# Optimization experiments

Hardware: AMD Instinct MI355X
Metric: run time of the kernel (lower is better)

The kernel has to match this reference:

```python
import jax, jax.numpy as jnp
import numpy as np

C = 1024        # BIGNET_DIM
GS = 128        # group_size
R = 4           # lora_dim
NL = 12         # 4 blocks x 3 QLoRALinear
N = 4096        # batch
NG = C * C // GS  # 8192 groups per layer
EPS = 1e-5


def dequant4(q4, norm):
    # q4: [NG, GS//2] int32 in [0,255] (two nibbles per byte), norm: [NG,1] f32
    low = q4 & 0xF
    high = (q4 >> 4) & 0xF
    # interleave: even positions = low nibble, odd = high nibble
    q8 = jnp.stack([low, high], axis=-1).reshape(q4.shape[0], GS)
    w = (q8.astype(jnp.float32) / 15.0 * 2.0 - 1.0) * norm
    return w.reshape(C, C)  # [out_features, in_features]


def qlora_linear(x, q4, norm, a, b):
    # base 4-bit dequant matmul + low-rank LoRA add (bias=False)
    w = dequant4(q4, norm)
    return x @ w.T + (x @ a.T) @ b.T  # [N,C]


def block(x, q4s, norms, As, Bs):
    h = qlora_linear(x, q4s[0], norms[0], As[0], Bs[0])
    h = jax.nn.relu(h)
    h = qlora_linear(h, q4s[1], norms[1], As[1], Bs[1])
    h = jax.nn.relu(h)
    h = qlora_linear(h, q4s[2], norms[2], As[2], Bs[2])
    return h + x  # residual


def layer_norm(x, g, b):
    mu = jnp.mean(x, axis=-1, keepdims=True)
    var = jnp.var(x, axis=-1, keepdims=True)
    return (x - mu) * jax.lax.rsqrt(var + EPS) * g + b


def setup_inputs() -> dict:
    key = jax.random.key(0)
    ks = jax.random.split(key, 5)
    x = jax.random.normal(ks[0], (N, C), dtype=jnp.float32)
    w_q4 = jax.random.randint(ks[1], (NL, NG, GS // 2), 0, 256, dtype=jnp.int32)
    w_norm = jax.random.uniform(ks[2], (NL, NG, 1), dtype=jnp.float32, minval=0.01, maxval=0.1)
    lora_a = jax.random.normal(ks[3], (NL, R, C), dtype=jnp.float32) * 0.02
    lora_b = jax.random.normal(ks[4], (NL, C, R), dtype=jnp.float32) * 0.02
    ln_g = jnp.ones((2, C), dtype=jnp.float32)
    ln_b = jnp.zeros((2, C), dtype=jnp.float32)
    return {"x": x, "w_q4": w_q4, "w_norm": w_norm, "lora_a": lora_a,
            "lora_b": lora_b, "ln_g": ln_g, "ln_b": ln_b}


def reference(x, w_q4, w_norm, lora_a, lora_b, ln_g, ln_b):
    h = block(x, w_q4[0:3], w_norm[0:3], lora_a[0:3], lora_b[0:3])
    h = layer_norm(h, ln_g[0], ln_b[0])
    h = block(h, w_q4[3:6], w_norm[3:6], lora_a[3:6], lora_b[3:6])
    h = block(h, w_q4[6:9], w_norm[6:9], lora_a[6:9], lora_b[6:9])
    h = layer_norm(h, ln_g[1], ln_b[1])
    h = block(h, w_q4[9:12], w_norm[9:12], lora_a[9:12], lora_b[9:12])
    return h
```

## Files before the change

### kernel.cpp

```cpp
#include <hip/hip_runtime.h>

#define CD 1024
#define NB 4096

typedef __attribute__((ext_vector_type(8))) short short8;
typedef __attribute__((ext_vector_type(4))) short short4v;
typedef __attribute__((ext_vector_type(4))) float f32x4;
typedef __attribute__((ext_vector_type(4))) int int4v;

typedef __attribute__((address_space(1))) const void gv_t;
typedef __attribute__((address_space(3))) void lv_t;
#define GLOAD16(g, l) __builtin_amdgcn_global_load_lds((gv_t*)(g), (lv_t*)(l), 16, 0, 0)

__device__ __forceinline__ short f2bf(float f) {
  unsigned u = __float_as_uint(f);
  u = (u + 0x7FFFu + ((u >> 16) & 1u)) >> 16;
  return (short)u;
}
__device__ __forceinline__ float bf2f(short s) {
  return __uint_as_float(((unsigned)(unsigned short)s) << 16);
}

__global__ __launch_bounds__(256) void prep_kernel(const float* __restrict__ x,
                                                   short* __restrict__ xb,
                                                   const int* __restrict__ q4,
                                                   const float* __restrict__ nrm,
                                                   const float* __restrict__ la,
                                                   const float* __restrict__ lb,
                                                   short* __restrict__ Wb) {
  int bid = blockIdx.x;
  if (bid < 2048) {
    int i = (bid * 256 + threadIdx.x) * 8;
    f32x4 a = *(const f32x4*)(x + i);
    f32x4 b = *(const f32x4*)(x + i + 4);
    short8 o;
    o[0] = f2bf(a[0]); o[1] = f2bf(a[1]); o[2] = f2bf(a[2]); o[3] = f2bf(a[3]);
    o[4] = f2bf(b[0]); o[5] = f2bf(b[1]); o[6] = f2bf(b[2]); o[7] = f2bf(b[3]);
    *(short8*)(xb + i) = o;
    return;
  }
  int tidg = (bid - 2048) * 256 + threadIdx.x;
  int w0 = tidg * 4;
  int l = w0 >> 19;
  int wl = w0 & 524287;
  int g = wl >> 6;
  int j0 = wl & 63;
  int o = g >> 3;
  int kb = ((g & 7) << 7) + (j0 << 1);
  int4v q = *(const int4v*)(q4 + w0);
  float n = nrm[(l << 13) + g];
  float s = n * (2.0f / 15.0f);
  f32x4 B = *(const f32x4*)(lb + (((l << 10) + o) << 2));
  const float* A = la + (l << 12);
  float Ar[4][8];
#pragma unroll
  for (int r = 0; r < 4; ++r) {
    f32x4 u = *(const f32x4*)(A + r * CD + kb);
    f32x4 v = *(const f32x4*)(A + r * CD + kb + 4);
    Ar[r][0] = u[0]; Ar[r][1] = u[1]; Ar[r][2] = u[2]; Ar[r][3] = u[3];
    Ar[r][4] = v[0]; Ar[r][5] = v[1]; Ar[r][6] = v[2]; Ar[r][7] = v[3];
  }
  short8 outv;
#pragma unroll
  for (int p = 0; p < 8; ++p) {
    int qw = q[p >> 1];
    int nib = (qw >> ((p & 1) << 2)) & 15;
    float wv = (float)nib * s - n;
    wv += B[0] * Ar[0][p] + B[1] * Ar[1][p] + B[2] * Ar[2][p] + B[3] * Ar[3][p];
    outv[p] = f2bf(wv);
  }
  *(short8*)(Wb + (l << 20) + (o << 10) + kb) = outv;
}

template <int EPI>
__global__ __launch_bounds__(256, 2) void qgemm(const short* __restrict__ Act,
                                                const short* __restrict__ W,
                                                const short* __restrict__ Res,
                                                void* __restrict__ Out) {
  __shared__ __align__(16) short ldsA[2][128 * 64];
  __shared__ __align__(16) short ldsB[2][64 * 64];
  const int tid = threadIdx.x;
  const int lane = tid & 63;
  const int wid = tid >> 6;
  const int wr = wid >> 1, wc = wid & 1;
  const int m0 = blockIdx.x * 128;
  const int o0 = blockIdx.y * 64;

  const int srow = tid >> 3;
  const int gch = (tid & 7) ^ (srow & 7);
  const short* abase = Act + (long)(m0 + srow) * CD + (gch << 3);
  const short* bbase = W + (long)(o0 + srow) * CD + (gch << 3);

  auto stage = [&](int t, int buf) {
    const int koff = t << 6;
#pragma unroll
    for (int i = 0; i < 4; ++i)
      GLOAD16(abase + ((long)(i << 5)) * CD + koff, &ldsA[buf][(tid + (i << 8)) << 3]);
#pragma unroll
    for (int i = 0; i < 2; ++i)
      GLOAD16(bbase + ((long)(i << 5)) * CD + koff, &ldsB[buf][(tid + (i << 8)) << 3]);
  };

  f32x4 acc[4][2] = {};
  const int frow = lane & 15;
  const int fch = lane >> 4;
  const int fsw = lane & 7;

  stage(0, 0);
  for (int t = 0; t < 16; ++t) {
    __syncthreads();
    if (t < 15) stage(t + 1, (t + 1) & 1);
    const short* La = ldsA[t & 1];
    const short* Lb = ldsB[t & 1];
#pragma unroll
    for (int kk = 0; kk < 2; ++kk) {
      const int chb = (kk << 2) + fch;
      short8 af[4], wf[2];
#pragma unroll
      for (int m = 0; m < 4; ++m) {
        int row = (wr << 6) + (m << 4) + frow;
        af[m] = *(const short8*)(La + (row << 6) + ((chb ^ fsw) << 3));
      }
#pragma unroll
      for (int n = 0; n < 2; ++n) {
        int row = (wc << 5) + (n << 4) + frow;
        wf[n] = *(const short8*)(Lb + (row << 6) + ((chb ^ fsw) << 3));
      }
#pragma unroll
      for (int m = 0; m < 4; ++m)
#pragma unroll
        for (int n = 0; n < 2; ++n)
          acc[m][n] = __builtin_amdgcn_mfma_f32_16x16x32_bf16(wf[n], af[m], acc[m][n], 0, 0, 0);
    }
  }

  const int orow = m0 + (wr << 6) + frow;
  const int ocol = o0 + (wc << 5) + (fch << 2);
#pragma unroll
  for (int m = 0; m < 4; ++m) {
#pragma unroll
    for (int n = 0; n < 2; ++n) {
      long row = orow + (m << 4);
      int col = ocol + (n << 4);
      f32x4 v = acc[m][n];
      if (EPI == 0) {
        short4v ov;
        ov[0] = f2bf(fmaxf(v[0], 0.0f));
        ov[1] = f2bf(fmaxf(v[1], 0.0f));
        ov[2] = f2bf(fmaxf(v[2], 0.0f));
        ov[3] = f2bf(fmaxf(v[3], 0.0f));
        *(short4v*)((short*)Out + row * CD + col) = ov;
      } else if (EPI == 2) {
        short4v rv = *(const short4v*)(Res + row * CD + col);
        short4v ov;
        ov[0] = f2bf(v[0] + bf2f(rv[0]));
        ov[1] = f2bf(v[1] + bf2f(rv[1]));
        ov[2] = f2bf(v[2] + bf2f(rv[2]));
        ov[3] = f2bf(v[3] + bf2f(rv[3]));
        *(short4v*)((short*)Out + row * CD + col) = ov;
      } else {
        short4v rv = *(const short4v*)(Res + row * CD + col);
        f32x4 ov;
        ov[0] = v[0] + bf2f(rv[0]);
        ov[1] = v[1] + bf2f(rv[1]);
        ov[2] = v[2] + bf2f(rv[2]);
        ov[3] = v[3] + bf2f(rv[3]);
        *(f32x4*)((float*)Out + row * CD + col) = ov;
      }
    }
  }
}

__global__ __launch_bounds__(256) void ln_kernel(const short* __restrict__ in,
                                                 short* __restrict__ out,
                                                 const float* __restrict__ g,
                                                 const float* __restrict__ b) {
  __shared__ float rs_[4], rq_[4];
  int row = blockIdx.x, tid = threadIdx.x;
  int k = tid * 4;
  short4v v = *(const short4v*)(in + (long)row * CD + k);
  float f0 = bf2f(v[0]), f1 = bf2f(v[1]), f2 = bf2f(v[2]), f3 = bf2f(v[3]);
  float s = f0 + f1 + f2 + f3;
  float q = f0 * f0 + f1 * f1 + f2 * f2 + f3 * f3;
#pragma unroll
  for (int off = 1; off < 64; off <<= 1) {
    s += __shfl_xor(s, off);
    q += __shfl_xor(q, off);
  }
  if ((tid & 63) == 0) { rs_[tid >> 6] = s; rq_[tid >> 6] = q; }
  __syncthreads();
  s = rs_[0] + rs_[1] + rs_[2] + rs_[3];
  q = rq_[0] + rq_[1] + rq_[2] + rq_[3];
  float mu = s * (1.0f / 1024.0f);
  float var = q * (1.0f / 1024.0f) - mu * mu;
  float rstd = rsqrtf(var + 1e-5f);
  short4v o;
  o[0] = f2bf((f0 - mu) * rstd * g[k] + b[k]);
  o[1] = f2bf((f1 - mu) * rstd * g[k + 1] + b[k + 1]);
  o[2] = f2bf((f2 - mu) * rstd * g[k + 2] + b[k + 2]);
  o[3] = f2bf((f3 - mu) * rstd * g[k + 3] + b[k + 3]);
  *(short4v*)(out + (long)row * CD + k) = o;
}

extern "C" void kernel_launch(void* const* d_in, const int* in_sizes, int n_in,
                              void* d_out, int out_size, void* d_ws, size_t ws_size,
                              hipStream_t stream) {
  const float* x = (const float*)d_in[0];
  const int* q4 = (const int*)d_in[1];
  const float* nrm = (const float*)d_in[2];
  const float* la = (const float*)d_in[3];
  const float* lb = (const float*)d_in[4];
  const float* lng = (const float*)d_in[5];
  const float* lnb = (const float*)d_in[6];

  short* Wb = (short*)d_ws;
  short* buf0 = (short*)((char*)d_ws + (24u << 20));
  short* buf1 = buf0 + (long)NB * CD;
  short* buf2 = (short*)d_out;
  short* buf3 = buf2 + (long)NB * CD;
  float* outf = (float*)d_out;

  prep_kernel<<<dim3(8192), dim3(256), 0, stream>>>(x, buf0, q4, nrm, la, lb, Wb);

  dim3 gg(32, 16), bb(256);
  auto Wl = [&](int l) { return Wb + ((long)l << 20); };

  qgemm<0><<<gg, bb, 0, stream>>>(buf0, Wl(0), nullptr, buf1);
  qgemm<0><<<gg, bb, 0, stream>>>(buf1, Wl(1), nullptr, buf2);
  qgemm<2><<<gg, bb, 0, stream>>>(buf2, Wl(2), buf0, buf3);
  ln_kernel<<<dim3(4096), dim3(256), 0, stream>>>(buf3, buf0, lng, lnb);
  qgemm<0><<<gg, bb, 0, stream>>>(buf0, Wl(3), nullptr, buf1);
  qgemm<0><<<gg, bb, 0, stream>>>(buf1, Wl(4), nullptr, buf2);
  qgemm<2><<<gg, bb, 0, stream>>>(buf2, Wl(5), buf0, buf3);
  qgemm<0><<<gg, bb, 0, stream>>>(buf3, Wl(6), nullptr, buf1);
  qgemm<0><<<gg, bb, 0, stream>>>(buf1, Wl(7), nullptr, buf2);
  qgemm<2><<<gg, bb, 0, stream>>>(buf2, Wl(8), buf3, buf0);
  ln_kernel<<<dim3(4096), dim3(256), 0, stream>>>(buf0, buf1, lng + CD, lnb + CD);
  qgemm<0><<<gg, bb, 0, stream>>>(buf1, Wl(9), nullptr, buf2);
  qgemm<0><<<gg, bb, 0, stream>>>(buf2, Wl(10), nullptr, buf0);
  qgemm<3><<<gg, bb, 0, stream>>>(buf0, Wl(11), buf1, (void*)outf);
}
```

Measured before the change: 322.4 us.

## Use 128x128 GEMM tiles with triple-buffered LDS and XCD-aware block mapping

Widens each workgroup's output tile from 128x64 to 128x128, which doubles MFMA work per LDS fragment load and halves the number of blocks. The K loop becomes a three-stage LDS ring with explicit vmcnt waits and raw s_barrier, so two tiles stay in flight ahead of the compute. A 1D grid is remapped so each XCD gets a contiguous group of M tiles for better L2 reuse. The trade-off is higher register and LDS use (96KB), which lowers occupancy, and a grid of 256 blocks that may leave CUs idle.

```diff
diff --git a/kernel.cpp b/kernel.cpp
--- a/kernel.cpp
+++ b/kernel.cpp
@@ -73,73 +73,87 @@
 }
 
 template <int EPI>
-__global__ __launch_bounds__(256, 2) void qgemm(const short* __restrict__ Act,
-                                                const short* __restrict__ W,
-                                                const short* __restrict__ Res,
-                                                void* __restrict__ Out) {
-  __shared__ __align__(16) short ldsA[2][128 * 64];
-  __shared__ __align__(16) short ldsB[2][64 * 64];
+__global__ __launch_bounds__(256) void qgemm(const short* __restrict__ Act,
+                                             const short* __restrict__ W,
+                                             const short* __restrict__ Res,
+                                             void* __restrict__ Out) {
+  __shared__ __align__(16) short ldsA[3][128 * 64];
+  __shared__ __align__(16) short ldsB[3][128 * 64];
   const int tid = threadIdx.x;
   const int lane = tid & 63;
   const int wid = tid >> 6;
   const int wr = wid >> 1, wc = wid & 1;
-  const int m0 = blockIdx.x * 128;
-  const int o0 = blockIdx.y * 64;
-
-  const int srow = tid >> 3;
-  const int gch = (tid & 7) ^ (srow & 7);
-  const short* abase = Act + (long)(m0 + srow) * CD + (gch << 3);
-  const short* bbase = W + (long)(o0 + srow) * CD + (gch << 3);
+  const int f = blockIdx.x;
+  const int xcd = f & 7, c = f >> 3;
+  const int m0 = (((xcd << 2) | (c & 3)) << 7);
+  const int o0 = ((c >> 2) << 7);
+
+  const int srow = (wid << 5) + (lane >> 3);
+  const int gch = (lane & 7) ^ (lane >> 3);
+  const short* aptr[4];
+  const short* bptr[4];
+#pragma unroll
+  for (int i = 0; i < 4; ++i) {
+    aptr[i] = Act + (long)(m0 + srow + (i << 3)) * CD + (gch << 3);
+    bptr[i] = W + (long)(o0 + srow + (i << 3)) * CD + (gch << 3);
+  }
 
   auto stage = [&](int t, int buf) {
     const int koff = t << 6;
 #pragma unroll
-    for (int i = 0; i < 4; ++i)
-      GLOAD16(abase + ((long)(i << 5)) * CD + koff, &ldsA[buf][(tid + (i << 8)) << 3]);
-#pragma unroll
-    for (int i = 0; i < 2; ++i)
-      GLOAD16(bbase + ((long)(i << 5)) * CD + koff, &ldsB[buf][(tid + (i << 8)) << 3]);
+    for (int i = 0; i < 4; ++i) {
+      GLOAD16(aptr[i] + koff, &ldsA[buf][((wid << 5) + (i << 3)) << 6]);
+      GLOAD16(bptr[i] + koff, &ldsB[buf][((wid << 5) + (i << 3)) << 6]);
+    }
   };
 
-  f32x4 acc[4][2] = {};
+  f32x4 acc[4][4] = {};
   const int frow = lane & 15;
   const int fch = lane >> 4;
   const int fsw = lane & 7;
 
   stage(0, 0);
+  stage(1, 1);
+  int cur = 0;
   for (int t = 0; t < 16; ++t) {
-    __syncthreads();
-    if (t < 15) stage(t + 1, (t + 1) & 1);
-    const short* La = ldsA[t & 1];
-    const short* Lb = ldsB[t & 1];
+    if (t < 15) asm volatile("s_waitcnt vmcnt(8)" ::: "memory");
+    else        asm volatile("s_waitcnt vmcnt(0)" ::: "memory");
+    asm volatile("s_waitcnt lgkmcnt(0)" ::: "memory");
+    __builtin_amdgcn_sched_barrier(0);
+    __builtin_amdgcn_s_barrier();
+    __builtin_amdgcn_sched_barrier(0);
+    if (t + 2 < 16) stage(t + 2, (cur == 0) ? 2 : cur - 1);
+    const short* La = ldsA[cur];
+    const short* Lb = ldsB[cur];
 #pragma unroll
     for (int kk = 0; kk < 2; ++kk) {
-      const int chb = (kk << 2) + fch;
-      short8 af[4], wf[2];
+      const int chsw = ((kk << 2) + fch) ^ fsw;
+      short8 af[4], wf[4];
 #pragma unroll
       for (int m = 0; m < 4; ++m) {
         int row = (wr << 6) + (m << 4) + frow;
-        af[m] = *(const short8*)(La + (row << 6) + ((chb ^ fsw) << 3));
+        af[m] = *(const short8*)(La + (row << 6) + (chsw << 3));
       }
 #pragma unroll
-      for (int n = 0; n < 2; ++n) {
-        int row = (wc << 5) + (n << 4) + frow;
-        wf[n] = *(const short8*)(Lb + (row << 6) + ((chb ^ fsw) << 3));
+      for (int n = 0; n < 4; ++n) {
+        int row = (wc << 6) + (n << 4) + frow;
+        wf[n] = *(const short8*)(Lb + (row << 6) + (chsw << 3));
       }
 #pragma unroll
       for (int m = 0; m < 4; ++m)
 #pragma unroll
-        for (int n = 0; n < 2; ++n)
+        for (int n = 0; n < 4; ++n)
           acc[m][n] = __builtin_amdgcn_mfma_f32_16x16x32_bf16(wf[n], af[m], acc[m][n], 0, 0, 0);
     }
+    cur = (cur == 2) ? 0 : cur + 1;
   }
 
   const int orow = m0 + (wr << 6) + frow;
-  const int ocol = o0 + (wc << 5) + (fch << 2);
+  const int ocol = o0 + (wc << 6) + (fch << 2);
 #pragma unroll
   for (int m = 0; m < 4; ++m) {
 #pragma unroll
-    for (int n = 0; n < 2; ++n) {
+    for (int n = 0; n < 4; ++n) {
       long row = orow + (m << 4);
       int col = ocol + (n << 4);
       f32x4 v = acc[m][n];
@@ -222,7 +236,7 @@
 
   prep_kernel<<<dim3(8192), dim3(256), 0, stream>>>(x, buf0, q4, nrm, la, lb, Wb);
 
-  dim3 gg(32, 16), bb(256);
+  dim3 gg(256), bb(256);
   auto Wl = [&](int l) { return Wb + ((long)l << 20); };
 
   qgemm<0><<<gg, bb, 0, stream>>>(buf0, Wl(0), nullptr, buf1);
```

After: 351.9 us. 1.09x slower.

## Restructure qgemm to 128x128 tiles with activations loaded straight into registers

Applied to the files above, without the earlier changes.

The GEMM kernel now uses 512-thread blocks computing 128x128 output tiles, with a flat 256-block grid remapped so blocks sharing rows land on the same XCD. Activation fragments are loaded directly from global memory into double-buffered registers instead of going through LDS. Only the weight tile is staged in LDS, using a triple-buffered async pipeline with manual vmcnt waits. The aim is to cut LDS traffic and sync overhead and to improve cache locality. In exchange it adds register pressure, uncoalesced-ish direct global loads for A, and fragile hand-counted waitcnts.

```diff
diff --git a/kernel.cpp b/kernel.cpp
--- a/kernel.cpp
+++ b/kernel.cpp
@@ -73,64 +73,83 @@
 }
 
 template <int EPI>
-__global__ __launch_bounds__(256, 2) void qgemm(const short* __restrict__ Act,
-                                                const short* __restrict__ W,
-                                                const short* __restrict__ Res,
-                                                void* __restrict__ Out) {
-  __shared__ __align__(16) short ldsA[2][128 * 64];
-  __shared__ __align__(16) short ldsB[2][64 * 64];
+__global__ __launch_bounds__(512) void qgemm(const short* __restrict__ Act,
+                                             const short* __restrict__ W,
+                                             const short* __restrict__ Res,
+                                             void* __restrict__ Out) {
+  __shared__ __align__(16) short ldsW[3][128 * 64];
   const int tid = threadIdx.x;
   const int lane = tid & 63;
   const int wid = tid >> 6;
-  const int wr = wid >> 1, wc = wid & 1;
-  const int m0 = blockIdx.x * 128;
-  const int o0 = blockIdx.y * 64;
-
-  const int srow = tid >> 3;
-  const int gch = (tid & 7) ^ (srow & 7);
-  const short* abase = Act + (long)(m0 + srow) * CD + (gch << 3);
-  const short* bbase = W + (long)(o0 + srow) * CD + (gch << 3);
-
-  auto stage = [&](int t, int buf) {
-    const int koff = t << 6;
-#pragma unroll
-    for (int i = 0; i < 4; ++i)
-      GLOAD16(abase + ((long)(i << 5)) * CD + koff, &ldsA[buf][(tid + (i << 8)) << 3]);
-#pragma unroll
-    for (int i = 0; i < 2; ++i)
-      GLOAD16(bbase + ((long)(i << 5)) * CD + koff, &ldsB[buf][(tid + (i << 8)) << 3]);
-  };
-
-  f32x4 acc[4][2] = {};
+  const int wr = wid >> 2;
+  const int wc = wid & 3;
+  const int f = blockIdx.x;
+  const int xcd = f & 7, c = f >> 3;
+  const int m0 = (((xcd << 2) | (c & 3)) << 7);
+  const int o0 = ((c >> 2) << 7);
+
   const int frow = lane & 15;
   const int fch = lane >> 4;
-  const int fsw = lane & 7;
-
-  stage(0, 0);
+
+  const int swrow = tid >> 3;
+  const short* wsrc0 = W + (long)(o0 + swrow) * CD + (((tid & 7) ^ (swrow & 7)) << 3);
+  const short* wsrc1 = W + (long)(o0 + swrow + 64) * CD + (((tid & 7) ^ ((swrow + 64) & 7)) << 3);
+
+  const short* arow[4];
+#pragma unroll
+  for (int m = 0; m < 4; ++m)
+    arow[m] = Act + (long)(m0 + (wr << 6) + (m << 4) + frow) * CD + (fch << 3);
+
+  f32x4 acc[4][2] = {};
+  short8 afA[8], afB[8];
+
+  auto stageW = [&](int T, int buf) {
+    const int koff = T << 6;
+    GLOAD16(wsrc0 + koff, &ldsW[buf][tid << 3]);
+    GLOAD16(wsrc1 + koff, &ldsW[buf][(tid + 512) << 3]);
+  };
+  auto loadA = [&](int T, short8* dst) {
+    const int c0 = T << 6;
+#pragma unroll
+    for (int kk = 0; kk < 2; ++kk)
+#pragma unroll
+      for (int m = 0; m < 4; ++m)
+        dst[kk * 4 + m] = *(const short8*)(arow[m] + c0 + (kk << 5));
+  };
+
+  stageW(0, 0);
+  stageW(1, 1);
+  loadA(0, afA);
+
+#pragma unroll
   for (int t = 0; t < 16; ++t) {
-    __syncthreads();
-    if (t < 15) stage(t + 1, (t + 1) & 1);
-    const short* La = ldsA[t & 1];
-    const short* Lb = ldsB[t & 1];
+    short8* cur = (t & 1) ? afB : afA;
+    short8* nxt = (t & 1) ? afA : afB;
+    if (t < 15) asm volatile("s_waitcnt vmcnt(10)" ::: "memory");
+    else        asm volatile("s_waitcnt vmcnt(8)" ::: "memory");
+    asm volatile("s_waitcnt lgkmcnt(0)" ::: "memory");
+    __builtin_amdgcn_sched_barrier(0);
+    __builtin_amdgcn_s_barrier();
+    __builtin_amdgcn_sched_barrier(0);
+    if (t + 1 < 16) loadA(t + 1, nxt);
+    __builtin_amdgcn_sched_barrier(0);
+    if (t + 2 < 16) stageW(t + 2, (t + 2) % 3);
+    __builtin_amdgcn_sched_barrier(0);
+    const short* Lw = ldsW[t % 3];
 #pragma unroll
     for (int kk = 0; kk < 2; ++kk) {
-      const int chb = (kk << 2) + fch;
-      short8 af[4], wf[2];
-#pragma unroll
-      for (int m = 0; m < 4; ++m) {
-        int row = (wr << 6) + (m << 4) + frow;
-        af[m] = *(const short8*)(La + (row << 6) + ((chb ^ fsw) << 3));
-      }
+      short8 wf[2];
 #pragma unroll
       for (int n = 0; n < 2; ++n) {
         int row = (wc << 5) + (n << 4) + frow;
-        wf[n] = *(const short8*)(Lb + (row << 6) + ((chb ^ fsw) << 3));
+        int ch = ((kk << 2) + fch) ^ (frow & 7);
+        wf[n] = *(const short8*)(Lw + (row << 6) + (ch << 3));
       }
 #pragma unroll
       for (int m = 0; m < 4; ++m)
 #pragma unroll
         for (int n = 0; n < 2; ++n)
-          acc[m][n] = __builtin_amdgcn_mfma_f32_16x16x32_bf16(wf[n], af[m], acc[m][n], 0, 0, 0);
+          acc[m][n] = __builtin_amdgcn_mfma_f32_16x16x32_bf16(wf[n], cur[kk * 4 + m], acc[m][n], 0, 0, 0);
     }
   }
 
@@ -222,7 +241,7 @@
 
   prep_kernel<<<dim3(8192), dim3(256), 0, stream>>>(x, buf0, q4, nrm, la, lb, Wb);
 
-  dim3 gg(32, 16), bb(256);
+  dim3 gg(256), bb(512);
   auto Wl = [&](int l) { return Wb + ((long)l << 20); };
 
   qgemm<0><<<gg, bb, 0, stream>>>(buf0, Wl(0), nullptr, buf1);
```

Measured after the change: 566.5 us. 1.76x slower.

## Enlarge GEMM tile to 128x128 with 512 threads, K-step 128, XCD-aware block mapping

Applied to the files above, without the earlier changes.

The bf16 GEMM goes from 128x64 tiles with 256 threads to 128x128 tiles with 8 waves per block, which raises operand reuse per byte loaded into LDS. The K step per stage doubles to 128 using two 64-wide swizzled LDS halves, so each GEMM needs half as many barriers. A 1D grid of 256 blocks is remapped so that each XCD's blocks share the same M rows, aiming at better L2 locality. In exchange the kernel uses 128KB of LDS per block, which lowers occupancy to about one block per CU, and launches only 256 blocks, exactly one wave of work on 256 CUs.

```diff
diff --git a/kernel.cpp b/kernel.cpp
--- a/kernel.cpp
+++ b/kernel.cpp
@@ -73,32 +73,44 @@
 }
 
 template <int EPI>
-__global__ __launch_bounds__(256, 2) void qgemm(const short* __restrict__ Act,
-                                                const short* __restrict__ W,
-                                                const short* __restrict__ Res,
-                                                void* __restrict__ Out) {
-  __shared__ __align__(16) short ldsA[2][128 * 64];
-  __shared__ __align__(16) short ldsB[2][64 * 64];
+__global__ __launch_bounds__(512) void qgemm(const short* __restrict__ Act,
+                                             const short* __restrict__ W,
+                                             const short* __restrict__ Res,
+                                             void* __restrict__ Out) {
+  __shared__ __align__(16) short ldsA[2][2][128 * 64];
+  __shared__ __align__(16) short ldsB[2][2][128 * 64];
   const int tid = threadIdx.x;
   const int lane = tid & 63;
   const int wid = tid >> 6;
-  const int wr = wid >> 1, wc = wid & 1;
-  const int m0 = blockIdx.x * 128;
-  const int o0 = blockIdx.y * 64;
-
-  const int srow = tid >> 3;
-  const int gch = (tid & 7) ^ (srow & 7);
-  const short* abase = Act + (long)(m0 + srow) * CD + (gch << 3);
-  const short* bbase = W + (long)(o0 + srow) * CD + (gch << 3);
+  const int wr = wid >> 2;
+  const int wc = wid & 3;
+  const int f = blockIdx.x;
+  const int xcd = f & 7, c = f >> 3;
+  const int m0 = (((xcd << 2) | (c & 3)) << 7);
+  const int o0 = ((c >> 2) << 7);
+
+  const short* aptr[2][2];
+  const short* bptr[2][2];
+#pragma unroll
+  for (int h = 0; h < 2; ++h)
+#pragma unroll
+    for (int i = 0; i < 2; ++i) {
+      int cc = tid + (i << 9);
+      int row = cc >> 3;
+      int ch = (cc & 7) ^ (row & 7);
+      aptr[h][i] = Act + (long)(m0 + row) * CD + (h << 6) + (ch << 3);
+      bptr[h][i] = W + (long)(o0 + row) * CD + (h << 6) + (ch << 3);
+    }
 
   auto stage = [&](int t, int buf) {
-    const int koff = t << 6;
-#pragma unroll
-    for (int i = 0; i < 4; ++i)
-      GLOAD16(abase + ((long)(i << 5)) * CD + koff, &ldsA[buf][(tid + (i << 8)) << 3]);
-#pragma unroll
-    for (int i = 0; i < 2; ++i)
-      GLOAD16(bbase + ((long)(i << 5)) * CD + koff, &ldsB[buf][(tid + (i << 8)) << 3]);
+    const int koff = t << 7;
+#pragma unroll
+    for (int h = 0; h < 2; ++h)
+#pragma unroll
+      for (int i = 0; i < 2; ++i) {
+        GLOAD16(aptr[h][i] + koff, &ldsA[buf][h][(tid + (i << 9)) << 3]);
+        GLOAD16(bptr[h][i] + koff, &ldsB[buf][h][(tid + (i << 9)) << 3]);
+      }
   };
 
   f32x4 acc[4][2] = {};
@@ -107,24 +119,24 @@
   const int fsw = lane & 7;
 
   stage(0, 0);
-  for (int t = 0; t < 16; ++t) {
+  for (int t = 0; t < 8; ++t) {
     __syncthreads();
-    if (t < 15) stage(t + 1, (t + 1) & 1);
-    const short* La = ldsA[t & 1];
-    const short* Lb = ldsB[t & 1];
-#pragma unroll
-    for (int kk = 0; kk < 2; ++kk) {
-      const int chb = (kk << 2) + fch;
+    if (t < 7) stage(t + 1, (t + 1) & 1);
+#pragma unroll
+    for (int kk = 0; kk < 4; ++kk) {
+      const short* La = ldsA[t & 1][kk >> 1];
+      const short* Lb = ldsB[t & 1][kk >> 1];
+      const int chsw = (((kk & 1) << 2) + fch) ^ fsw;
       short8 af[4], wf[2];
 #pragma unroll
       for (int m = 0; m < 4; ++m) {
         int row = (wr << 6) + (m << 4) + frow;
-        af[m] = *(const short8*)(La + (row << 6) + ((chb ^ fsw) << 3));
+        af[m] = *(const short8*)(La + (row << 6) + (chsw << 3));
       }
 #pragma unroll
       for (int n = 0; n < 2; ++n) {
         int row = (wc << 5) + (n << 4) + frow;
-        wf[n] = *(const short8*)(Lb + (row << 6) + ((chb ^ fsw) << 3));
+        wf[n] = *(const short8*)(Lb + (row << 6) + (chsw << 3));
       }
 #pragma unroll
       for (int m = 0; m < 4; ++m)
@@ -222,7 +234,7 @@
 
   prep_kernel<<<dim3(8192), dim3(256), 0, stream>>>(x, buf0, q4, nrm, la, lb, Wb);
 
-  dim3 gg(32, 16), bb(256);
+  dim3 gg(256), bb(512);
   auto Wl = [&](int l) { return Wb + ((long)l << 20); };
 
   qgemm<0><<<gg, bb, 0, stream>>>(buf0, Wl(0), nullptr, buf1);
```

Result: faster. 278.9 us (-13.5%).
